# Optimization experiments

Hardware: AMD Instinct MI355X
Metric: run time of the kernel (lower is better)

## Reference

```python
import jax, jax.numpy as jnp
import numpy as np

B, C, H, W = 2, 64, 96, 96

def setup_inputs() -> dict:
    key = jax.random.key(0)
    k1, k2 = jax.random.split(key)
    feature_yi = jax.random.normal(k1, (B, C, H, W), dtype=jnp.float32)
    feature_pi = jax.random.normal(k2, (B, C, H, W), dtype=jnp.float32)
    return {"feature_yi": feature_yi, "feature_pi": feature_pi}

def reference(feature_yi, feature_pi):
    b, c, h, w = feature_yi.shape
    yi = feature_yi.reshape(b, c, h * w)  # [B, C, M]
    pi = feature_pi.reshape(b, c, h * w)  # [B, C, N]
    # scores[b, m, n] = sum_c yi[b,c,m] * pi[b,c,n]
    scores = jnp.einsum('bcm,bcn->bmn', yi, pi)
    # softmax over dim=1 (query axis m), as in the torch code
    weight = jax.nn.softmax(scores, axis=1)  # [B, M, N]
    # attention_output[b, c, n] = sum_m yi[b,c,m] * weight[b,m,n]
    out = jnp.einsum('bcm,bmn->bcn', yi, weight)
    return out.reshape(b, c, h, w)
```

## Files before the change

kernel.cpp:

```cpp
#include <hip/hip_runtime.h>
#include <hip/hip_bf16.h>


#define CC 64
#define MM 9216
#define BB 2
#define WAVES 4
#define NPW 32
#define NBLK (WAVES * NPW)
#define NBX (MM / NBLK)
#define MTILE 64
#define NT (MM / MTILE)

typedef __bf16 bf16x8 __attribute__((ext_vector_type(8)));
typedef float f32x16 __attribute__((ext_vector_type(16)));
typedef unsigned int u32x4 __attribute__((ext_vector_type(4)));

__device__ __forceinline__ int swz(int r) { return ((r >> 1) ^ (r >> 4)) & 7; }

__device__ __forceinline__ void gld16(const void* gsrc, void* ldst) {
    __builtin_amdgcn_global_load_lds(
        (const __attribute__((address_space(1))) void*)gsrc,
        (__attribute__((address_space(3))) void*)ldst, 16, 0, 0);
}

__device__ __forceinline__ float fexp2(float x) {
#if __has_builtin(__builtin_amdgcn_exp2f)
    return __builtin_amdgcn_exp2f(x);
#else
    return exp2f(x);
#endif
}

__device__ __forceinline__ unsigned int pack2(float a, float b) {
    const unsigned short ua = __builtin_bit_cast(unsigned short, (__bf16)a);
    const unsigned short ub = __builtin_bit_cast(unsigned short, (__bf16)b);
    return (unsigned int)ua | ((unsigned int)ub << 16);
}

__global__ __launch_bounds__(256)
void prepass(const float* __restrict__ yi, __bf16* __restrict__ kt,
             __bf16* __restrict__ vt)
{
    const int t    = blockIdx.x >> 1;
    const int half = blockIdx.x & 1;
    const int b    = blockIdx.y;
    const int tsk  = half * 256 + threadIdx.x;
    const float* src = yi + (size_t)b * CC * MM;

    {
        const int m = tsk & 63, g = tsk >> 6;
        const int m_abs = t * 64 + m;
        bf16x8 hh;
        #pragma unroll
        for (int j = 0; j < 8; ++j)
            hh[j] = (__bf16)src[(size_t)(g * 8 + j) * MM + m_abs];
        *reinterpret_cast<bf16x8*>(
            kt + (size_t)(b * MM + m_abs) * 64 + ((g ^ swz(m)) << 3)) = hh;
    }
    {
        const int c = tsk & 63, gm = tsk >> 6;
        const float* p = src + (size_t)c * MM + t * 64 + gm * 8;
        bf16x8 hh;
        #pragma unroll
        for (int j = 0; j < 8; ++j) hh[j] = (__bf16)p[j];
        *reinterpret_cast<bf16x8*>(
            vt + (size_t)(b * CC + c) * MM + t * 64 + ((gm ^ swz(c)) << 3)) = hh;
    }
}

template<bool FINAL>
__global__ __launch_bounds__(WAVES * 64, 2)
void attn_main(const __bf16* __restrict__ kt, const __bf16* __restrict__ vt,
               const float* __restrict__ pi,
               float* __restrict__ out, float* __restrict__ opart,
               float* __restrict__ lpart, const int nsplits)
{
    __shared__ __align__(16) __bf16 k_sm[2][MTILE][64];
    __shared__ __align__(16) __bf16 v_sm[2][CC][64];

    const int tid  = threadIdx.x;
    const int lane = tid & 63;
    const int wave = tid >> 6;
    const int l31  = lane & 31;
    const int hi   = lane >> 5;

    int bx, split, b;
    if (gridDim.y == 1 && !FINAL) {
        const int bid = blockIdx.x;
        const int xcd = bid & 7, slot = bid >> 3;
        bx = slot % NBX;
        const int g = xcd + 8 * (slot / NBX);
        split = g % nsplits;
        b     = g / nsplits;
    } else {
        bx = blockIdx.x; split = blockIdx.y; b = blockIdx.z;
    }

    const int tpb = NT / nsplits;
    const int t0s = split * tpb;
    const int n0  = bx * NBLK + wave * NPW;
    const int n_g = n0 + l31;

    const __bf16* gq[4];
    char* ld0[4];
    char* ld1[4];
    int gstep[4];
    #pragma unroll
    for (int q = 0; q < 4; ++q) {
        const int ch = wave * 4 + q;
        if (ch < 8) {
            gq[q]    = kt + (size_t)(b * MM + t0s * 64) * 64 + ch * 512 + lane * 8;
            gstep[q] = MTILE * 64;
            ld0[q]   = (char*)(&k_sm[0][0][0]) + ch * 1024;
            ld1[q]   = (char*)(&k_sm[1][0][0]) + ch * 1024;
        } else {
            const int j = ch - 8;
            const int c = j * 8 + (lane >> 3);
            gq[q]    = vt + (size_t)(b * CC + c) * MM + t0s * 64 + (lane & 7) * 8;
            gstep[q] = MTILE;
            ld0[q]   = (char*)(&v_sm[0][0][0]) + j * 1024;
            ld1[q]   = (char*)(&v_sm[1][0][0]) + j * 1024;
        }
    }
    auto stage = [&](int bb) {
        #pragma unroll
        for (int q = 0; q < 4; ++q) {
            gld16(gq[q], bb ? ld1[q] : ld0[q]);
            gq[q] += gstep[q];
        }
    };

    stage(0);

    const float LOG2E = 1.4426950408889634f;
    bf16x8 qh[4], ql[4];
    {
        const float* qb = pi + (size_t)b * CC * MM + n_g;
        #pragma unroll
        for (int ks = 0; ks < 4; ++ks)
            #pragma unroll
            for (int j = 0; j < 8; ++j) {
                const float f = qb[(size_t)(ks * 16 + hi * 8 + j) * MM] * LOG2E;
                const __bf16 h = (__bf16)f;
                qh[ks][j] = h;
                ql[ks][j] = (__bf16)(f - (float)h);
            }
    }

    f32x16 o0, o1;
    #pragma unroll
    for (int r = 0; r < 16; ++r) { o0[r] = 0.f; o1[r] = 0.f; }
    float run_l = 0.f;

    const int sx0 = swz(l31) << 3;
    const int sx1 = swz(32 + l31) << 3;

    __syncthreads();
    int buf = 0;

    for (int it = 0; it < tpb; ++it) {
        if (it + 1 < tpb) stage(buf ^ 1);

        f32x16 s0, s1;
        #pragma unroll
        for (int r = 0; r < 16; ++r) { s0[r] = 0.f; s1[r] = 0.f; }
        __builtin_amdgcn_s_setprio(1);
        #pragma unroll
        for (int ks = 0; ks < 4; ++ks) {
            const int cb = ks * 16 + hi * 8;
            const bf16x8 a0 = *(const bf16x8*)&k_sm[buf][l31][cb ^ sx0];
            const bf16x8 a1 = *(const bf16x8*)&k_sm[buf][32 + l31][cb ^ sx1];
            s0 = __builtin_amdgcn_mfma_f32_32x32x16_bf16(a0, qh[ks], s0, 0, 0, 0);
            s1 = __builtin_amdgcn_mfma_f32_32x32x16_bf16(a1, qh[ks], s1, 0, 0, 0);
            s0 = __builtin_amdgcn_mfma_f32_32x32x16_bf16(a0, ql[ks], s0, 0, 0, 0);
            s1 = __builtin_amdgcn_mfma_f32_32x32x16_bf16(a1, ql[ks], s1, 0, 0, 0);
        }
        __builtin_amdgcn_s_setprio(0);

        float ps[8];
        #pragma unroll
        for (int r = 0; r < 8; ++r) {
            s0[r]     = fexp2(s0[r]);
            s0[r + 8] = fexp2(s0[r + 8]);
            s1[r]     = fexp2(s1[r]);
            s1[r + 8] = fexp2(s1[r + 8]);
            ps[r] = (s0[r] + s0[r + 8]) + (s1[r] + s1[r + 8]);
        }
        float psum = ((ps[0] + ps[1]) + (ps[2] + ps[3])) +
                     ((ps[4] + ps[5]) + (ps[6] + ps[7]));
        psum += __shfl_xor(psum, 32);
        run_l += psum;

        unsigned int X[2][4][2];
        #pragma unroll
        for (int q = 0; q < 4; ++q)
            #pragma unroll
            for (int d = 0; d < 2; ++d) {
                X[0][q][d] = pack2(s0[4 * q + 2 * d], s0[4 * q + 2 * d + 1]);
                X[1][q][d] = pack2(s1[4 * q + 2 * d], s1[4 * q + 2 * d + 1]);
            }

        __builtin_amdgcn_s_setprio(1);
        #pragma unroll
        for (int ks = 0; ks < 4; ++ks) {
            const int mt = ks >> 1, e = ks & 1;
            auto rA = __builtin_amdgcn_permlane32_swap(
                X[mt][2 * e][0], X[mt][2 * e + 1][0], false, false);
            auto rB = __builtin_amdgcn_permlane32_swap(
                X[mt][2 * e][1], X[mt][2 * e + 1][1], false, false);
            u32x4 w;
            w.x = rA[0];
            w.y = rB[0];
            w.z = rA[1];
            w.w = rB[1];
            const bf16x8 bp = __builtin_bit_cast(bf16x8, w);

            const int cb = ks * 16 + hi * 8;
            const bf16x8 av0 = *(const bf16x8*)&v_sm[buf][l31][cb ^ sx0];
            const bf16x8 av1 = *(const bf16x8*)&v_sm[buf][32 + l31][cb ^ sx1];
            o0 = __builtin_amdgcn_mfma_f32_32x32x16_bf16(av0, bp, o0, 0, 0, 0);
            o1 = __builtin_amdgcn_mfma_f32_32x32x16_bf16(av1, bp, o1, 0, 0, 0);
        }
        __builtin_amdgcn_s_setprio(0);

        __syncthreads();
        buf ^= 1;
    }

    if (FINAL) {
        const float inv = 1.f / run_l;
        #pragma unroll
        for (int r = 0; r < 16; ++r) {
            const int cl = (r & 3) + 8 * (r >> 2) + 4 * hi;
            out[((size_t)b * CC + cl) * MM + n_g]      = o0[r] * inv;
            out[((size_t)b * CC + cl + 32) * MM + n_g] = o1[r] * inv;
        }
    } else {
        const size_t pbase = (size_t)(b * nsplits + split) * CC * MM;
        #pragma unroll
        for (int r = 0; r < 16; ++r) {
            const int cl = (r & 3) + 8 * (r >> 2) + 4 * hi;
            opart[pbase + (size_t)cl * MM + n_g]        = o0[r];
            opart[pbase + (size_t)(cl + 32) * MM + n_g] = o1[r];
        }
        if (hi == 0)
            lpart[(size_t)(b * nsplits + split) * MM + n_g] = run_l;
    }
}

template<int S>
__global__ __launch_bounds__(256)
void attn_reduce4(const float* __restrict__ opart, const float* __restrict__ lpart,
                  float* __restrict__ out)
{
    const int t = blockIdx.x * 256 + threadIdx.x;
    if (t >= BB * CC * MM / 4) return;
    const int n  = (t * 4) % MM;
    const int bc = (t * 4) / MM;
    const int b  = bc / CC;
    const int c  = bc - b * CC;

    float L[4]   = {0.f, 0.f, 0.f, 0.f};
    float acc[4] = {0.f, 0.f, 0.f, 0.f};
    #pragma unroll
    for (int s = 0; s < S; ++s) {
        const float4 l4 = *reinterpret_cast<const float4*>(
            &lpart[(size_t)(b * S + s) * MM + n]);
        L[0] += l4.x; L[1] += l4.y; L[2] += l4.z; L[3] += l4.w;
        const float4 o4 = *reinterpret_cast<const float4*>(
            &opart[((size_t)(b * S + s) * CC + c) * MM + n]);
        acc[0] += o4.x; acc[1] += o4.y; acc[2] += o4.z; acc[3] += o4.w;
    }
    float4 r;
    r.x = acc[0] / L[0]; r.y = acc[1] / L[1];
    r.z = acc[2] / L[2]; r.w = acc[3] / L[3];
    *reinterpret_cast<float4*>(&out[(size_t)t * 4]) = r;
}

extern "C" void kernel_launch(void* const* d_in, const int* in_sizes, int n_in,
                              void* d_out, int out_size, void* d_ws, size_t ws_size,
                              hipStream_t stream) {
    const float* yi = (const float*)d_in[0];
    const float* pi = (const float*)d_in[1];
    float* out = (float*)d_out;

    const size_t kelems = (size_t)BB * MM * 64;
    const size_t velems = (size_t)BB * CC * MM;
    const size_t preB   = (kelems + velems) * 2;
    auto need = [&](int s) -> size_t {
        return preB + (size_t)BB * s * CC * MM * 4 + (size_t)BB * s * MM * 4;
    };

    int S = 1;
    if (d_ws) {
        if (ws_size >= need(8))      S = 8;
        else if (ws_size >= need(4)) S = 4;
        else if (ws_size >= need(2)) S = 2;
    }

    if (S == 1) {
        if (!d_ws || ws_size < preB) return;
        __bf16* kt = (__bf16*)d_ws;
        __bf16* vt = kt + kelems;
        prepass<<<dim3(NT * 2, BB), dim3(256), 0, stream>>>(yi, kt, vt);
        attn_main<true><<<dim3(NBX, 1, BB), dim3(WAVES * 64), 0, stream>>>(
            kt, vt, pi, out, out, out, 1);
        return;
    }

    __bf16* kt   = (__bf16*)d_ws;
    __bf16* vt   = kt + kelems;
    float* opart = (float*)(vt + velems);
    float* lp    = opart + (size_t)BB * S * CC * MM;

    prepass<<<dim3(NT * 2, BB), dim3(256), 0, stream>>>(yi, kt, vt);

    if (S == 8) {
        attn_main<false><<<dim3(NBX * 2 * S), dim3(WAVES * 64), 0, stream>>>(
            kt, vt, pi, out, opart, lp, S);
    } else {
        attn_main<false><<<dim3(NBX, S, BB), dim3(WAVES * 64), 0, stream>>>(
            kt, vt, pi, out, opart, lp, S);
    }

    const int total4 = BB * CC * MM / 4;
    const dim3 rg((total4 + 255) / 256), rb(256);
    if (S == 8)      attn_reduce4<8><<<rg, rb, 0, stream>>>(opart, lp, out);
    else if (S == 4) attn_reduce4<4><<<rg, rb, 0, stream>>>(opart, lp, out);
    else             attn_reduce4<2><<<rg, rb, 0, stream>>>(opart, lp, out);
}
```

Baseline: 91.40 us.

## Raise occupancy to four blocks per CU by cutting register pressure

Raises the launch-bounds minimum blocks per CU from 2 to 4. To fit the tighter register budget it computes the two 32-row score halves one after another, keeping only one f32x16 score accumulator live, and replaces the per-chunk stage step and second-buffer pointer arrays with a single stride and a fixed buffer offset. The aim is more resident waves to hide global-to-LDS and MFMA latency. The cost is less instruction-level parallelism between the two MFMA chains and a risk of register spills under the stricter bound.

```diff
diff --git a/kernel.cpp b/kernel.cpp
--- a/kernel.cpp
+++ b/kernel.cpp
@@ -70,7 +70,7 @@
 }
 
 template<bool FINAL>
-__global__ __launch_bounds__(WAVES * 64, 2)
+__global__ __launch_bounds__(WAVES * 64, 4)
 void attn_main(const __bf16* __restrict__ kt, const __bf16* __restrict__ vt,
                const float* __restrict__ pi,
                float* __restrict__ out, float* __restrict__ opart,
@@ -102,32 +102,29 @@
     const int n0  = bx * NBLK + wave * NPW;
     const int n_g = n0 + l31;
 
+    const bool iskt = (wave < 2);
+    const int  gstep = iskt ? (MTILE * 64) : MTILE;
     const __bf16* gq[4];
     char* ld0[4];
-    char* ld1[4];
-    int gstep[4];
     #pragma unroll
     for (int q = 0; q < 4; ++q) {
         const int ch = wave * 4 + q;
-        if (ch < 8) {
-            gq[q]    = kt + (size_t)(b * MM + t0s * 64) * 64 + ch * 512 + lane * 8;
-            gstep[q] = MTILE * 64;
-            ld0[q]   = (char*)(&k_sm[0][0][0]) + ch * 1024;
-            ld1[q]   = (char*)(&k_sm[1][0][0]) + ch * 1024;
+        if (iskt) {
+            gq[q]  = kt + (size_t)(b * MM + t0s * 64) * 64 + ch * 512 + lane * 8;
+            ld0[q] = (char*)(&k_sm[0][0][0]) + ch * 1024;
         } else {
             const int j = ch - 8;
             const int c = j * 8 + (lane >> 3);
-            gq[q]    = vt + (size_t)(b * CC + c) * MM + t0s * 64 + (lane & 7) * 8;
-            gstep[q] = MTILE;
-            ld0[q]   = (char*)(&v_sm[0][0][0]) + j * 1024;
-            ld1[q]   = (char*)(&v_sm[1][0][0]) + j * 1024;
+            gq[q]  = vt + (size_t)(b * CC + c) * MM + t0s * 64 + (lane & 7) * 8;
+            ld0[q] = (char*)(&v_sm[0][0][0]) + j * 1024;
         }
     }
     auto stage = [&](int bb) {
+        const int off = bb ? 8192 : 0;
         #pragma unroll
         for (int q = 0; q < 4; ++q) {
-            gld16(gq[q], bb ? ld1[q] : ld0[q]);
-            gq[q] += gstep[q];
+            gld16(gq[q], ld0[q] + off);
+            gq[q] += gstep;
         }
     };
 
@@ -162,44 +159,42 @@
     for (int it = 0; it < tpb; ++it) {
         if (it + 1 < tpb) stage(buf ^ 1);
 
-        f32x16 s0, s1;
-        #pragma unroll
-        for (int r = 0; r < 16; ++r) { s0[r] = 0.f; s1[r] = 0.f; }
-        __builtin_amdgcn_s_setprio(1);
-        #pragma unroll
-        for (int ks = 0; ks < 4; ++ks) {
-            const int cb = ks * 16 + hi * 8;
-            const bf16x8 a0 = *(const bf16x8*)&k_sm[buf][l31][cb ^ sx0];
-            const bf16x8 a1 = *(const bf16x8*)&k_sm[buf][32 + l31][cb ^ sx1];
-            s0 = __builtin_amdgcn_mfma_f32_32x32x16_bf16(a0, qh[ks], s0, 0, 0, 0);
-            s1 = __builtin_amdgcn_mfma_f32_32x32x16_bf16(a1, qh[ks], s1, 0, 0, 0);
-            s0 = __builtin_amdgcn_mfma_f32_32x32x16_bf16(a0, ql[ks], s0, 0, 0, 0);
-            s1 = __builtin_amdgcn_mfma_f32_32x32x16_bf16(a1, ql[ks], s1, 0, 0, 0);
-        }
-        __builtin_amdgcn_s_setprio(0);
-
-        float ps[8];
-        #pragma unroll
-        for (int r = 0; r < 8; ++r) {
-            s0[r]     = fexp2(s0[r]);
-            s0[r + 8] = fexp2(s0[r + 8]);
-            s1[r]     = fexp2(s1[r]);
-            s1[r + 8] = fexp2(s1[r + 8]);
-            ps[r] = (s0[r] + s0[r + 8]) + (s1[r] + s1[r + 8]);
-        }
-        float psum = ((ps[0] + ps[1]) + (ps[2] + ps[3])) +
-                     ((ps[4] + ps[5]) + (ps[6] + ps[7]));
+        unsigned int X[2][4][2];
+        float psum = 0.f;
+        #pragma unroll
+        for (int h = 0; h < 2; ++h) {
+            const int sxh = h ? sx1 : sx0;
+            const int row = h * 32 + l31;
+            f32x16 s;
+            #pragma unroll
+            for (int r = 0; r < 16; ++r) s[r] = 0.f;
+            __builtin_amdgcn_s_setprio(1);
+            #pragma unroll
+            for (int ks = 0; ks < 4; ++ks) {
+                const int cb = ks * 16 + hi * 8;
+                const bf16x8 a = *(const bf16x8*)&k_sm[buf][row][cb ^ sxh];
+                s = __builtin_amdgcn_mfma_f32_32x32x16_bf16(a, qh[ks], s, 0, 0, 0);
+                s = __builtin_amdgcn_mfma_f32_32x32x16_bf16(a, ql[ks], s, 0, 0, 0);
+            }
+            __builtin_amdgcn_s_setprio(0);
+
+            float ps[8];
+            #pragma unroll
+            for (int r = 0; r < 8; ++r) {
+                s[r]     = fexp2(s[r]);
+                s[r + 8] = fexp2(s[r + 8]);
+                ps[r] = s[r] + s[r + 8];
+            }
+            psum += ((ps[0] + ps[1]) + (ps[2] + ps[3])) +
+                    ((ps[4] + ps[5]) + (ps[6] + ps[7]));
+            #pragma unroll
+            for (int q = 0; q < 4; ++q)
+                #pragma unroll
+                for (int d = 0; d < 2; ++d)
+                    X[h][q][d] = pack2(s[4 * q + 2 * d], s[4 * q + 2 * d + 1]);
+        }
         psum += __shfl_xor(psum, 32);
         run_l += psum;
-
-        unsigned int X[2][4][2];
-        #pragma unroll
-        for (int q = 0; q < 4; ++q)
-            #pragma unroll
-            for (int d = 0; d < 2; ++d) {
-                X[0][q][d] = pack2(s0[4 * q + 2 * d], s0[4 * q + 2 * d + 1]);
-                X[1][q][d] = pack2(s1[4 * q + 2 * d], s1[4 * q + 2 * d + 1]);
-            }
 
         __builtin_amdgcn_s_setprio(1);
         #pragma unroll
```

New measurement: 190.7 us. 109% more time.
